# Kernel tuning notes

Hardware: AMD Instinct MI355X
Metric: run time of the kernel (lower is better)

The kernel has to match this reference:

```python
import jax, jax.numpy as jnp
import numpy as np

EPS = 1e-05


def setup_inputs() -> dict:
    key = jax.random.key(0)
    k1, k2, k3 = jax.random.split(key, 3)
    B, T, D = 64, 2048, 768
    outputs = jax.random.normal(k1, (B, T, D), dtype=jnp.float32)
    lens = jax.random.uniform(k2, (B,), dtype=jnp.float32)  # fraction of valid frames
    gnoise_raw = jax.random.normal(k3, (B, D), dtype=jnp.float32)
    return {"outputs": outputs, "lens": lens, "gnoise_raw": gnoise_raw}


def reference(outputs, lens, gnoise_raw):
    # outputs: [B, T, D], lens: [B] (fraction), gnoise_raw: [B, D]
    B, T, D = outputs.shape
    length = lens * T  # float frame counts
    trunc = jnp.floor(length).astype(jnp.int32)  # torch int() truncation (lens > 0)
    count = jnp.clip(trunc + 1, 1, T)            # slice :int(length)+1 -> count frames
    # masked mean over the first `count` frames of each row (single fused pass)
    mask = (jnp.arange(T)[None, :] < count[:, None]).astype(outputs.dtype)  # [B, T]
    masked_mean = jnp.einsum('btd,bt->bd', outputs, mask) / count[:, None].astype(outputs.dtype)
    full_mean = outputs.mean(axis=1)  # used when length == 1
    mean = jnp.where((length != 1.0)[:, None], masked_mean, full_mean)  # [B, D]
    # gaussian noise normalized to [0,1] then scaled: eps*((1-9)*g + 9)
    g = gnoise_raw - jnp.min(gnoise_raw)
    g = g / jnp.max(g)
    gnoise = EPS * ((1.0 - 9.0) * g + 9.0)
    return (mean + gnoise)[:, None, :]  # [B, 1, D]
```

## Files before the change

kernel.cpp:

```cpp
#include <hip/hip_runtime.h>
#include <math.h>

#define B_ 64
#define T_ 2048
#define D_ 768
#define D4_ (D_ / 4)
#define S_ 16
#define CHUNK_ (T_ / S_)
#define EPS_ 1e-5f

static __device__ __forceinline__ int row_count(float lenfrac) {
    float length = lenfrac * (float)T_;
    if (length == 1.0f) return T_;
    int c = (int)floorf(length) + 1;
    if (c < 1) c = 1;
    if (c > T_) c = T_;
    return c;
}

__global__ __launch_bounds__(1024) void minmax_kernel(const float* __restrict__ g,
                                                      float* __restrict__ ws) {
    __shared__ float smin[16], smax[16];
    const int tid = threadIdx.x;
    float vmin = INFINITY, vmax = -INFINITY;
    const float4* g4 = (const float4*)g;
    const int n4 = B_ * D_ / 4;
    for (int i = tid; i < n4; i += 1024) {
        float4 v = g4[i];
        vmin = fminf(vmin, fminf(fminf(v.x, v.y), fminf(v.z, v.w)));
        vmax = fmaxf(vmax, fmaxf(fmaxf(v.x, v.y), fmaxf(v.z, v.w)));
    }
    #pragma unroll
    for (int off = 32; off >= 1; off >>= 1) {
        vmin = fminf(vmin, __shfl_down(vmin, off, 64));
        vmax = fmaxf(vmax, __shfl_down(vmax, off, 64));
    }
    const int wave = tid >> 6;
    if ((tid & 63) == 0) { smin[wave] = vmin; smax[wave] = vmax; }
    __syncthreads();
    if (tid < 64) {
        vmin = smin[tid & 15];
        vmax = smax[tid & 15];
        #pragma unroll
        for (int off = 8; off >= 1; off >>= 1) {
            vmin = fminf(vmin, __shfl_down(vmin, off, 64));
            vmax = fmaxf(vmax, __shfl_down(vmax, off, 64));
        }
        if (tid == 0) { ws[0] = vmin; ws[1] = vmax; }
    }
}

__global__ __launch_bounds__(192) void partial_kernel(const float* __restrict__ outp,
                                                      const float* __restrict__ lens,
                                                      float* __restrict__ partial) {
    const int b = blockIdx.x;
    const int s = blockIdx.y;
    const int tid = threadIdx.x;
    const int tcount = row_count(lens[b]);
    const int t0 = s * CHUNK_;
    const int t1 = min(t0 + CHUNK_, tcount);

    const float4* base = (const float4*)(outp + (size_t)b * T_ * D_) + tid;
    float4 a0 = {0.f, 0.f, 0.f, 0.f}, a1 = a0, a2 = a0, a3 = a0;
    int t = t0;
    for (; t + 3 < t1; t += 4) {
        float4 v0 = base[(size_t)(t + 0) * D4_];
        float4 v1 = base[(size_t)(t + 1) * D4_];
        float4 v2 = base[(size_t)(t + 2) * D4_];
        float4 v3 = base[(size_t)(t + 3) * D4_];
        a0.x += v0.x; a0.y += v0.y; a0.z += v0.z; a0.w += v0.w;
        a1.x += v1.x; a1.y += v1.y; a1.z += v1.z; a1.w += v1.w;
        a2.x += v2.x; a2.y += v2.y; a2.z += v2.z; a2.w += v2.w;
        a3.x += v3.x; a3.y += v3.y; a3.z += v3.z; a3.w += v3.w;
    }
    for (; t < t1; ++t) {
        float4 v0 = base[(size_t)t * D4_];
        a0.x += v0.x; a0.y += v0.y; a0.z += v0.z; a0.w += v0.w;
    }
    float4 acc;
    acc.x = (a0.x + a1.x) + (a2.x + a3.x);
    acc.y = (a0.y + a1.y) + (a2.y + a3.y);
    acc.z = (a0.z + a1.z) + (a2.z + a3.z);
    acc.w = (a0.w + a1.w) + (a2.w + a3.w);

    float4* p = (float4*)partial + ((size_t)s * B_ + b) * D4_ + tid;
    *p = acc;
}

__global__ __launch_bounds__(256) void finalize_kernel(const float* __restrict__ lens,
                                                       const float* __restrict__ graw,
                                                       const float* __restrict__ partial,
                                                       const float* __restrict__ mmws,
                                                       float* __restrict__ outp) {
    const int idx = blockIdx.x * 256 + threadIdx.x;
    if (idx >= B_ * D4_) return;
    const int b = idx / D4_;
    const int c4 = idx - b * D4_;

    const float4* part4 = (const float4*)partial;
    float4 acc = {0.f, 0.f, 0.f, 0.f};
    #pragma unroll
    for (int s = 0; s < S_; ++s) {
        float4 v = part4[((size_t)s * B_ + b) * D4_ + c4];
        acc.x += v.x; acc.y += v.y; acc.z += v.z; acc.w += v.w;
    }
    const float inv = 1.0f / (float)row_count(lens[b]);

    const float mn = mmws[0];
    const float mx = mmws[1];
    const float scale = 1.0f / (mx - mn);
    float4 g = ((const float4*)graw)[idx];
    float4 o;
    o.x = acc.x * inv + EPS_ * (9.0f - 8.0f * ((g.x - mn) * scale));
    o.y = acc.y * inv + EPS_ * (9.0f - 8.0f * ((g.y - mn) * scale));
    o.z = acc.z * inv + EPS_ * (9.0f - 8.0f * ((g.z - mn) * scale));
    o.w = acc.w * inv + EPS_ * (9.0f - 8.0f * ((g.w - mn) * scale));
    ((float4*)outp)[idx] = o;
}

extern "C" void kernel_launch(void* const* d_in, const int* in_sizes, int n_in,
                              void* d_out, int out_size, void* d_ws, size_t ws_size,
                              hipStream_t stream) {
    const float* outputs = (const float*)d_in[0];
    const float* lens    = (const float*)d_in[1];
    const float* graw    = (const float*)d_in[2];
    float* out = (float*)d_out;
    float* ws  = (float*)d_ws;

    float* partial = ws + 64;

    minmax_kernel<<<1, 1024, 0, stream>>>(graw, ws);
    partial_kernel<<<dim3(B_, S_), 192, 0, stream>>>(outputs, lens, partial);
    const int n4 = B_ * D4_;
    finalize_kernel<<<(n4 + 255) / 256, 256, 0, stream>>>(lens, graw, partial, ws, out);
}
```

Baseline: 483.5 us.

## Interleave time rows across more split blocks and fold min/max into finalize

```diff
diff --git a/kernel.cpp b/kernel.cpp
--- a/kernel.cpp
+++ b/kernel.cpp
@@ -4,9 +4,8 @@
 #define B_ 64
 #define T_ 2048
 #define D_ 768
-#define D4_ (D_ / 4)
-#define S_ 16
-#define CHUNK_ (T_ / S_)
+#define D4_ 192
+#define S_ 32
 #define EPS_ 1e-5f
 
 static __device__ __forceinline__ int row_count(float lenfrac) {
@@ -18,38 +17,6 @@
     return c;
 }
 
-__global__ __launch_bounds__(1024) void minmax_kernel(const float* __restrict__ g,
-                                                      float* __restrict__ ws) {
-    __shared__ float smin[16], smax[16];
-    const int tid = threadIdx.x;
-    float vmin = INFINITY, vmax = -INFINITY;
-    const float4* g4 = (const float4*)g;
-    const int n4 = B_ * D_ / 4;
-    for (int i = tid; i < n4; i += 1024) {
-        float4 v = g4[i];
-        vmin = fminf(vmin, fminf(fminf(v.x, v.y), fminf(v.z, v.w)));
-        vmax = fmaxf(vmax, fmaxf(fmaxf(v.x, v.y), fmaxf(v.z, v.w)));
-    }
-    #pragma unroll
-    for (int off = 32; off >= 1; off >>= 1) {
-        vmin = fminf(vmin, __shfl_down(vmin, off, 64));
-        vmax = fmaxf(vmax, __shfl_down(vmax, off, 64));
-    }
-    const int wave = tid >> 6;
-    if ((tid & 63) == 0) { smin[wave] = vmin; smax[wave] = vmax; }
-    __syncthreads();
-    if (tid < 64) {
-        vmin = smin[tid & 15];
-        vmax = smax[tid & 15];
-        #pragma unroll
-        for (int off = 8; off >= 1; off >>= 1) {
-            vmin = fminf(vmin, __shfl_down(vmin, off, 64));
-            vmax = fmaxf(vmax, __shfl_down(vmax, off, 64));
-        }
-        if (tid == 0) { ws[0] = vmin; ws[1] = vmax; }
-    }
-}
-
 __global__ __launch_bounds__(192) void partial_kernel(const float* __restrict__ outp,
                                                       const float* __restrict__ lens,
                                                       float* __restrict__ partial) {
@@ -57,23 +24,21 @@
     const int s = blockIdx.y;
     const int tid = threadIdx.x;
     const int tcount = row_count(lens[b]);
-    const int t0 = s * CHUNK_;
-    const int t1 = min(t0 + CHUNK_, tcount);
 
-    const float4* base = (const float4*)(outp + (size_t)b * T_ * D_) + tid;
+    const float4* base = (const float4*)(outp + (size_t)b * (T_ * D_)) + tid;
     float4 a0 = {0.f, 0.f, 0.f, 0.f}, a1 = a0, a2 = a0, a3 = a0;
-    int t = t0;
-    for (; t + 3 < t1; t += 4) {
-        float4 v0 = base[(size_t)(t + 0) * D4_];
-        float4 v1 = base[(size_t)(t + 1) * D4_];
-        float4 v2 = base[(size_t)(t + 2) * D4_];
-        float4 v3 = base[(size_t)(t + 3) * D4_];
+    int t = s;
+    for (; t + 3 * S_ < tcount; t += 4 * S_) {
+        float4 v0 = base[(size_t)t * D4_];
+        float4 v1 = base[(size_t)(t + S_) * D4_];
+        float4 v2 = base[(size_t)(t + 2 * S_) * D4_];
+        float4 v3 = base[(size_t)(t + 3 * S_) * D4_];
         a0.x += v0.x; a0.y += v0.y; a0.z += v0.z; a0.w += v0.w;
         a1.x += v1.x; a1.y += v1.y; a1.z += v1.z; a1.w += v1.w;
         a2.x += v2.x; a2.y += v2.y; a2.z += v2.z; a2.w += v2.w;
         a3.x += v3.x; a3.y += v3.y; a3.z += v3.z; a3.w += v3.w;
     }
-    for (; t < t1; ++t) {
+    for (; t < tcount; t += S_) {
         float4 v0 = base[(size_t)t * D4_];
         a0.x += v0.x; a0.y += v0.y; a0.z += v0.z; a0.w += v0.w;
     }
@@ -90,31 +55,47 @@
 __global__ __launch_bounds__(256) void finalize_kernel(const float* __restrict__ lens,
                                                        const float* __restrict__ graw,
                                                        const float* __restrict__ partial,
-                                                       const float* __restrict__ mmws,
                                                        float* __restrict__ outp) {
-    const int idx = blockIdx.x * 256 + threadIdx.x;
-    if (idx >= B_ * D4_) return;
+    const int tid = threadIdx.x;
+    const int idx = blockIdx.x * 256 + tid;
+
+    const float4* g4 = (const float4*)graw;
+    float vmin = INFINITY, vmax = -INFINITY;
+    for (int i = tid; i < B_ * D4_; i += 256) {
+        float4 v = g4[i];
+        vmin = fminf(vmin, fminf(fminf(v.x, v.y), fminf(v.z, v.w)));
+        vmax = fmaxf(vmax, fmaxf(fmaxf(v.x, v.y), fmaxf(v.z, v.w)));
+    }
+    #pragma unroll
+    for (int off = 1; off < 64; off <<= 1) {
+        vmin = fminf(vmin, __shfl_xor(vmin, off, 64));
+        vmax = fmaxf(vmax, __shfl_xor(vmax, off, 64));
+    }
+    __shared__ float red[8];
+    const int wave = tid >> 6;
+    if ((tid & 63) == 0) { red[wave] = vmin; red[4 + wave] = vmax; }
+    __syncthreads();
+    vmin = fminf(fminf(red[0], red[1]), fminf(red[2], red[3]));
+    vmax = fmaxf(fmaxf(red[4], red[5]), fmaxf(red[6], red[7]));
+    const float scale = 1.0f / (vmax - vmin);
+
     const int b = idx / D4_;
     const int c4 = idx - b * D4_;
-
-    const float4* part4 = (const float4*)partial;
+    const float4* p4 = (const float4*)partial;
     float4 acc = {0.f, 0.f, 0.f, 0.f};
     #pragma unroll
     for (int s = 0; s < S_; ++s) {
-        float4 v = part4[((size_t)s * B_ + b) * D4_ + c4];
+        float4 v = p4[((size_t)s * B_ + b) * D4_ + c4];
         acc.x += v.x; acc.y += v.y; acc.z += v.z; acc.w += v.w;
     }
     const float inv = 1.0f / (float)row_count(lens[b]);
 
-    const float mn = mmws[0];
-    const float mx = mmws[1];
-    const float scale = 1.0f / (mx - mn);
-    float4 g = ((const float4*)graw)[idx];
+    float4 g = g4[idx];
     float4 o;
-    o.x = acc.x * inv + EPS_ * (9.0f - 8.0f * ((g.x - mn) * scale));
-    o.y = acc.y * inv + EPS_ * (9.0f - 8.0f * ((g.y - mn) * scale));
-    o.z = acc.z * inv + EPS_ * (9.0f - 8.0f * ((g.z - mn) * scale));
-    o.w = acc.w * inv + EPS_ * (9.0f - 8.0f * ((g.w - mn) * scale));
+    o.x = acc.x * inv + EPS_ * (9.0f - 8.0f * ((g.x - vmin) * scale));
+    o.y = acc.y * inv + EPS_ * (9.0f - 8.0f * ((g.y - vmin) * scale));
+    o.z = acc.z * inv + EPS_ * (9.0f - 8.0f * ((g.z - vmin) * scale));
+    o.w = acc.w * inv + EPS_ * (9.0f - 8.0f * ((g.w - vmin) * scale));
     ((float4*)outp)[idx] = o;
 }
 
@@ -125,12 +106,8 @@
     const float* lens    = (const float*)d_in[1];
     const float* graw    = (const float*)d_in[2];
     float* out = (float*)d_out;
-    float* ws  = (float*)d_ws;
+    float* partial = (float*)d_ws;
 
-    float* partial = ws + 64;
-
-    minmax_kernel<<<1, 1024, 0, stream>>>(graw, ws);
     partial_kernel<<<dim3(B_, S_), 192, 0, stream>>>(outputs, lens, partial);
-    const int n4 = B_ * D4_;
-    finalize_kernel<<<(n4 + 255) / 256, 256, 0, stream>>>(lens, graw, partial, ws, out);
+    finalize_kernel<<<48, 256, 0, stream>>>(lens, graw, partial, out);
 }
```

Result: slower. 495.7 us (+2.5%).
